# Performance work log

Measured on AMD Instinct MI355X. Metric: run time of the kernel, lower is better.

Reference implementation:

```python
import jax, jax.numpy as jnp
import numpy as np

INPUT_SIZE = 1024
HIDDEN_SIZE = 1024
BATCH = 4096


def setup_inputs() -> dict:
    key = jax.random.key(0)
    ks = jax.random.split(key, 16)
    s_in = 1.0 / np.sqrt(INPUT_SIZE)
    s_h = 1.0 / np.sqrt(HIDDEN_SIZE)
    inp = {
        "incoming": jax.random.normal(ks[0], (BATCH, INPUT_SIZE), jnp.float32),
        "old_h": jax.random.normal(ks[1], (BATCH, HIDDEN_SIZE), jnp.float32),
        "old_c": jax.random.normal(ks[2], (BATCH, HIDDEN_SIZE), jnp.float32),
    }
    # torch nn.Linear weights: [out, in]; y = x @ W.T + b
    names = ["i", "o", "f", "c"]
    for j, n in enumerate(names):
        inp[f"w_{n}"] = jax.random.normal(ks[3 + 3 * j], (HIDDEN_SIZE, INPUT_SIZE), jnp.float32) * s_in
        inp[f"b_{n}"] = jax.random.normal(ks[4 + 3 * j], (HIDDEN_SIZE,), jnp.float32) * s_in
        inp[f"u_{n}"] = jax.random.normal(ks[5 + 3 * j], (HIDDEN_SIZE, HIDDEN_SIZE), jnp.float32) * s_h
    return inp


def reference(incoming, old_h, old_c, w_i, b_i, u_i, w_o, b_o, u_o, w_f, b_f, u_f, w_c, b_c, u_c):
    # Concatenate the 4 input->gate and 4 hidden->gate matrices into two
    # fused GEMMs (same math as the 8 separate Linear calls).
    W = jnp.concatenate([w_i, w_o, w_f, w_c], axis=0)   # [4H, I]
    U = jnp.concatenate([u_i, u_o, u_f, u_c], axis=0)   # [4H, H]
    b = jnp.concatenate([b_i, b_o, b_f, b_c], axis=0)   # [4H]
    gates = incoming @ W.T + old_h @ U.T + b            # [B, 4H]
    gi, go, gf, gc = jnp.split(gates, 4, axis=-1)
    i = jax.nn.sigmoid(gi)
    o = jax.nn.sigmoid(go)
    f = jax.nn.sigmoid(gf)
    c_tilde = jnp.tanh(gc)
    new_c = f * old_c + i * c_tilde
    new_h = o * jnp.tanh(new_c)
    return (new_h, new_c)
```

## Files before the change

### kernel.cpp

```cpp
#include <hip/hip_runtime.h>

typedef __bf16 bf16x8 __attribute__((ext_vector_type(8)));
typedef float f32x4 __attribute__((ext_vector_type(4)));

#define B_  4096
#define IN_ 1024
#define H_  1024
#define KD  2048
#define ND  4096

__device__ __forceinline__ unsigned short f2bf(float f) {
    union { float f; unsigned u; } v; v.f = f;
    unsigned r = v.u + 0x7FFFu + ((v.u >> 16) & 1u);
    return (unsigned short)(r >> 16);
}
__device__ __forceinline__ float bf2f(unsigned short u) {
    union { unsigned u; float f; } v; v.u = ((unsigned)u) << 16; return v.f;
}

__global__ __launch_bounds__(256) void pack_z(const float* __restrict__ x,
                                              const float* __restrict__ h,
                                              unsigned short* __restrict__ Z) {
    int idx = (blockIdx.x * 256 + threadIdx.x) * 4;
    int m = idx >> 11;
    int k = idx & (KD - 1);
    const float* src = (k < IN_) ? (x + (size_t)m * IN_ + k)
                                 : (h + (size_t)m * H_ + (k - IN_));
    float4 v = *(const float4*)src;
    ushort4 o;
    o.x = f2bf(v.x); o.y = f2bf(v.y); o.z = f2bf(v.z); o.w = f2bf(v.w);
    *(ushort4*)(Z + idx) = o;
}

__global__ __launch_bounds__(256) void pack_v(const float* __restrict__ wi, const float* __restrict__ ui,
                                              const float* __restrict__ wo, const float* __restrict__ uo,
                                              const float* __restrict__ wf, const float* __restrict__ uf,
                                              const float* __restrict__ wc, const float* __restrict__ uc,
                                              unsigned short* __restrict__ V) {
    int idx = (blockIdx.x * 256 + threadIdx.x) * 4;
    int n = idx >> 11;
    int k = idx & (KD - 1);
    int g = n >> 10;
    int r = n & (H_ - 1);
    const float* wg = (g == 0) ? wi : (g == 1) ? wo : (g == 2) ? wf : wc;
    const float* ug = (g == 0) ? ui : (g == 1) ? uo : (g == 2) ? uf : uc;
    const float* src = (k < IN_) ? (wg + (size_t)r * IN_ + k)
                                 : (ug + (size_t)r * H_ + (k - IN_));
    float4 v = *(const float4*)src;
    ushort4 o;
    o.x = f2bf(v.x); o.y = f2bf(v.y); o.z = f2bf(v.z); o.w = f2bf(v.w);
    *(ushort4*)(V + idx) = o;
}

__global__ __launch_bounds__(256) void gemm_bt(const unsigned short* __restrict__ Z,
                                               const unsigned short* __restrict__ V,
                                               unsigned short* __restrict__ G) {
    __shared__ unsigned short lA[128 * 64];
    __shared__ unsigned short lB[128 * 64];
    const int tid  = threadIdx.x;
    const int lane = tid & 63;
    const int w    = tid >> 6;
    const int wr   = w >> 1;
    const int wc   = w & 1;
    const int m0   = blockIdx.y * 128;
    const int n0   = blockIdx.x * 128;

    f32x4 acc[4][4];
#pragma unroll
    for (int i = 0; i < 4; ++i)
#pragma unroll
        for (int j = 0; j < 4; ++j) acc[i][j] = (f32x4){0.f, 0.f, 0.f, 0.f};

    const int lr = lane >> 3;
    const int lc = (lane & 7) * 8;
    const unsigned short* gA = Z + (size_t)(m0 + w * 32 + lr) * KD + lc;
    const unsigned short* gB = V + (size_t)(n0 + w * 32 + lr) * KD + lc;
    unsigned short* lAw = lA + w * 32 * 64;
    unsigned short* lBw = lB + w * 32 * 64;

    const int lm = lane & 15;
    const int kq = (lane >> 4) * 8;

    for (int k0 = 0; k0 < KD; k0 += 64) {
#pragma unroll
        for (int c = 0; c < 4; ++c) {
            __builtin_amdgcn_global_load_lds(
                (const __attribute__((address_space(1))) void*)(gA + (size_t)c * 8 * KD + k0),
                (__attribute__((address_space(3))) void*)(lAw + c * 512), 16, 0, 0);
            __builtin_amdgcn_global_load_lds(
                (const __attribute__((address_space(1))) void*)(gB + (size_t)c * 8 * KD + k0),
                (__attribute__((address_space(3))) void*)(lBw + c * 512), 16, 0, 0);
        }
        __syncthreads();
#pragma unroll
        for (int ks = 0; ks < 2; ++ks) {
            bf16x8 af[4], bf[4];
            const int kb = ks * 32 + kq;
#pragma unroll
            for (int i = 0; i < 4; ++i) {
                af[i] = *(const bf16x8*)(lA + (wr * 64 + i * 16 + lm) * 64 + kb);
                bf[i] = *(const bf16x8*)(lB + (wc * 64 + i * 16 + lm) * 64 + kb);
            }
#pragma unroll
            for (int mi = 0; mi < 4; ++mi)
#pragma unroll
                for (int ni = 0; ni < 4; ++ni)
                    acc[mi][ni] = __builtin_amdgcn_mfma_f32_16x16x32_bf16(
                        af[mi], bf[ni], acc[mi][ni], 0, 0, 0);
        }
        __syncthreads();
    }

#pragma unroll
    for (int mi = 0; mi < 4; ++mi)
#pragma unroll
        for (int ni = 0; ni < 4; ++ni)
#pragma unroll
            for (int v = 0; v < 4; ++v) {
                int row = m0 + wr * 64 + mi * 16 + (lane >> 4) * 4 + v;
                int col = n0 + wc * 64 + ni * 16 + lm;
                G[(size_t)row * ND + col] = f2bf(acc[mi][ni][v]);
            }
}

__global__ __launch_bounds__(256) void lstm_elt(const unsigned short* __restrict__ G,
                                                const float* __restrict__ oc,
                                                const float* __restrict__ bi,
                                                const float* __restrict__ bo,
                                                const float* __restrict__ bff,
                                                const float* __restrict__ bc,
                                                float* __restrict__ nh,
                                                float* __restrict__ nc) {
    int idx = (blockIdx.x * 256 + threadIdx.x) * 4;
    int m = idx >> 10;
    int h = idx & (H_ - 1);
    size_t gb = (size_t)m * ND + h;
    ushort4 g0 = *(const ushort4*)(G + gb);
    ushort4 g1 = *(const ushort4*)(G + gb + 1024);
    ushort4 g2 = *(const ushort4*)(G + gb + 2048);
    ushort4 g3 = *(const ushort4*)(G + gb + 3072);
    float4 vbi = *(const float4*)(bi + h);
    float4 vbo = *(const float4*)(bo + h);
    float4 vbf = *(const float4*)(bff + h);
    float4 vbc = *(const float4*)(bc + h);
    float4 voc = *(const float4*)(oc + idx);
    float4 rh, rc;
#define COMP(c_)                                                         \
    {                                                                    \
        float gi = bf2f(g0.c_) + vbi.c_;                                 \
        float go = bf2f(g1.c_) + vbo.c_;                                 \
        float gf = bf2f(g2.c_) + vbf.c_;                                 \
        float gc = bf2f(g3.c_) + vbc.c_;                                 \
        float iv = 1.f / (1.f + __expf(-gi));                            \
        float ov = 1.f / (1.f + __expf(-go));                            \
        float fv = 1.f / (1.f + __expf(-gf));                            \
        float ct = 1.f - 2.f / (__expf(2.f * gc) + 1.f);                 \
        float cv = fv * voc.c_ + iv * ct;                                \
        float th = 1.f - 2.f / (__expf(2.f * cv) + 1.f);                 \
        rc.c_ = cv; rh.c_ = ov * th;                                     \
    }
    COMP(x) COMP(y) COMP(z) COMP(w)
#undef COMP
    *(float4*)(nh + idx) = rh;
    *(float4*)(nc + idx) = rc;
}

extern "C" void kernel_launch(void* const* d_in, const int* in_sizes, int n_in,
                              void* d_out, int out_size, void* d_ws, size_t ws_size,
                              hipStream_t stream) {
    const float* incoming = (const float*)d_in[0];
    const float* old_h    = (const float*)d_in[1];
    const float* old_c    = (const float*)d_in[2];
    const float* w_i = (const float*)d_in[3];
    const float* b_i = (const float*)d_in[4];
    const float* u_i = (const float*)d_in[5];
    const float* w_o = (const float*)d_in[6];
    const float* b_o = (const float*)d_in[7];
    const float* u_o = (const float*)d_in[8];
    const float* w_f = (const float*)d_in[9];
    const float* b_f = (const float*)d_in[10];
    const float* u_f = (const float*)d_in[11];
    const float* w_c = (const float*)d_in[12];
    const float* b_c = (const float*)d_in[13];
    const float* u_c = (const float*)d_in[14];

    unsigned short* Z = (unsigned short*)d_ws;
    unsigned short* V = Z + (size_t)B_ * KD;
    unsigned short* G = V + (size_t)ND * KD;

    pack_z<<<(B_ * KD / 4) / 256, 256, 0, stream>>>(incoming, old_h, Z);
    pack_v<<<((size_t)ND * KD / 4) / 256, 256, 0, stream>>>(
        w_i, u_i, w_o, u_o, w_f, u_f, w_c, u_c, V);
    gemm_bt<<<dim3(ND / 128, B_ / 128), 256, 0, stream>>>(Z, V, G);
    lstm_elt<<<(B_ * H_ / 4) / 256, 256, 0, stream>>>(
        G, old_c, b_i, b_o, b_f, b_c,
        (float*)d_out, (float*)d_out + (size_t)B_ * H_);
}
```

Before: 248.6 us.

## Fuse LSTM gate epilogue into GEMM with interleaved weight rows and LDS swizzle

Reorders the packed weight matrix so the four gates for each hidden unit sit in adjacent columns. The GEMM epilogue can then exchange accumulators across lanes with shuffles and compute new_h and new_c directly. This removes the bf16 gate buffer write and read and the separate elementwise launch. An XOR swizzle on the LDS tile layout is also added to cut bank conflicts on fragment reads. The tradeoffs are uncoalesced scalar old_c loads and output stores in the epilogue, plus extra shuffle work.

Measured after the change: 227.4 us. -8.5%, faster.

```diff
diff --git a/kernel.cpp b/kernel.cpp
--- a/kernel.cpp
+++ b/kernel.cpp
@@ -13,9 +13,6 @@
     union { float f; unsigned u; } v; v.f = f;
     unsigned r = v.u + 0x7FFFu + ((v.u >> 16) & 1u);
     return (unsigned short)(r >> 16);
-}
-__device__ __forceinline__ float bf2f(unsigned short u) {
-    union { unsigned u; float f; } v; v.u = ((unsigned)u) << 16; return v.f;
 }
 
 __global__ __launch_bounds__(256) void pack_z(const float* __restrict__ x,
@@ -40,8 +37,8 @@
     int idx = (blockIdx.x * 256 + threadIdx.x) * 4;
     int n = idx >> 11;
     int k = idx & (KD - 1);
-    int g = n >> 10;
-    int r = n & (H_ - 1);
+    int g = n & 3;
+    int r = n >> 2;
     const float* wg = (g == 0) ? wi : (g == 1) ? wo : (g == 2) ? wf : wc;
     const float* ug = (g == 0) ? ui : (g == 1) ? uo : (g == 2) ? uf : uc;
     const float* src = (k < IN_) ? (wg + (size_t)r * IN_ + k)
@@ -52,9 +49,15 @@
     *(ushort4*)(V + idx) = o;
 }
 
-__global__ __launch_bounds__(256) void gemm_bt(const unsigned short* __restrict__ Z,
-                                               const unsigned short* __restrict__ V,
-                                               unsigned short* __restrict__ G) {
+__global__ __launch_bounds__(256) void gemm_lstm(const unsigned short* __restrict__ Z,
+                                                 const unsigned short* __restrict__ V,
+                                                 const float* __restrict__ oc,
+                                                 const float* __restrict__ bi,
+                                                 const float* __restrict__ bo,
+                                                 const float* __restrict__ bff,
+                                                 const float* __restrict__ bc,
+                                                 float* __restrict__ nh,
+                                                 float* __restrict__ nc) {
     __shared__ unsigned short lA[128 * 64];
     __shared__ unsigned short lB[128 * 64];
     const int tid  = threadIdx.x;
@@ -72,7 +75,7 @@
         for (int j = 0; j < 4; ++j) acc[i][j] = (f32x4){0.f, 0.f, 0.f, 0.f};
 
     const int lr = lane >> 3;
-    const int lc = (lane & 7) * 8;
+    const int lc = ((lane & 7) ^ lr) * 8;
     const unsigned short* gA = Z + (size_t)(m0 + w * 32 + lr) * KD + lc;
     const unsigned short* gB = V + (size_t)(n0 + w * 32 + lr) * KD + lc;
     unsigned short* lAw = lA + w * 32 * 64;
@@ -95,11 +98,12 @@
 #pragma unroll
         for (int ks = 0; ks < 2; ++ks) {
             bf16x8 af[4], bf[4];
-            const int kb = ks * 32 + kq;
+            const int cb = ks * 4 + (lane >> 4);
+            const int sw = (cb ^ (lm & 7)) * 8;
 #pragma unroll
             for (int i = 0; i < 4; ++i) {
-                af[i] = *(const bf16x8*)(lA + (wr * 64 + i * 16 + lm) * 64 + kb);
-                bf[i] = *(const bf16x8*)(lB + (wc * 64 + i * 16 + lm) * 64 + kb);
+                af[i] = *(const bf16x8*)(lA + (wr * 64 + i * 16 + lm) * 64 + sw);
+                bf[i] = *(const bf16x8*)(lB + (wc * 64 + i * 16 + lm) * 64 + sw);
             }
 #pragma unroll
             for (int mi = 0; mi < 4; ++mi)
@@ -111,58 +115,43 @@
         __syncthreads();
     }
 
+    const int a  = lane >> 4;
+    const int b  = (lane >> 2) & 3;
+    const int g  = lane & 3;
+    const int h0 = blockIdx.x * 32 + wc * 16;
+    const int rowb = m0 + wr * 64 + 4 * a + g;
+
 #pragma unroll
-    for (int mi = 0; mi < 4; ++mi)
+    for (int ni = 0; ni < 4; ++ni) {
+        const int h = h0 + ni * 4 + b;
+        const float vbi = bi[h];
+        const float vbo = bo[h];
+        const float vbf = bff[h];
+        const float vbc = bc[h];
 #pragma unroll
-        for (int ni = 0; ni < 4; ++ni)
+        for (int mi = 0; mi < 4; ++mi) {
+            float recv[4];
 #pragma unroll
-            for (int v = 0; v < 4; ++v) {
-                int row = m0 + wr * 64 + mi * 16 + (lane >> 4) * 4 + v;
-                int col = n0 + wc * 64 + ni * 16 + lm;
-                G[(size_t)row * ND + col] = f2bf(acc[mi][ni][v]);
+            for (int t = 0; t < 4; ++t) {
+                float x = acc[mi][ni][(g ^ t) & 3];
+                recv[t] = __shfl_xor(x, t, 64);
             }
-}
-
-__global__ __launch_bounds__(256) void lstm_elt(const unsigned short* __restrict__ G,
-                                                const float* __restrict__ oc,
-                                                const float* __restrict__ bi,
-                                                const float* __restrict__ bo,
-                                                const float* __restrict__ bff,
-                                                const float* __restrict__ bc,
-                                                float* __restrict__ nh,
-                                                float* __restrict__ nc) {
-    int idx = (blockIdx.x * 256 + threadIdx.x) * 4;
-    int m = idx >> 10;
-    int h = idx & (H_ - 1);
-    size_t gb = (size_t)m * ND + h;
-    ushort4 g0 = *(const ushort4*)(G + gb);
-    ushort4 g1 = *(const ushort4*)(G + gb + 1024);
-    ushort4 g2 = *(const ushort4*)(G + gb + 2048);
-    ushort4 g3 = *(const ushort4*)(G + gb + 3072);
-    float4 vbi = *(const float4*)(bi + h);
-    float4 vbo = *(const float4*)(bo + h);
-    float4 vbf = *(const float4*)(bff + h);
-    float4 vbc = *(const float4*)(bc + h);
-    float4 voc = *(const float4*)(oc + idx);
-    float4 rh, rc;
-#define COMP(c_)                                                         \
-    {                                                                    \
-        float gi = bf2f(g0.c_) + vbi.c_;                                 \
-        float go = bf2f(g1.c_) + vbo.c_;                                 \
-        float gf = bf2f(g2.c_) + vbf.c_;                                 \
-        float gc = bf2f(g3.c_) + vbc.c_;                                 \
-        float iv = 1.f / (1.f + __expf(-gi));                            \
-        float ov = 1.f / (1.f + __expf(-go));                            \
-        float fv = 1.f / (1.f + __expf(-gf));                            \
-        float ct = 1.f - 2.f / (__expf(2.f * gc) + 1.f);                 \
-        float cv = fv * voc.c_ + iv * ct;                                \
-        float th = 1.f - 2.f / (__expf(2.f * cv) + 1.f);                 \
-        rc.c_ = cv; rh.c_ = ov * th;                                     \
+            float gi = recv[g] + vbi;
+            float go = recv[g ^ 1] + vbo;
+            float gf = recv[g ^ 2] + vbf;
+            float gc = recv[g ^ 3] + vbc;
+            const int row = rowb + mi * 16;
+            const size_t off = (size_t)row * H_ + h;
+            float iv = 1.f / (1.f + __expf(-gi));
+            float ov = 1.f / (1.f + __expf(-go));
+            float fv = 1.f / (1.f + __expf(-gf));
+            float ct = 1.f - 2.f / (__expf(2.f * gc) + 1.f);
+            float cv = fv * oc[off] + iv * ct;
+            float th = 1.f - 2.f / (__expf(2.f * cv) + 1.f);
+            nc[off] = cv;
+            nh[off] = ov * th;
+        }
     }
-    COMP(x) COMP(y) COMP(z) COMP(w)
-#undef COMP
-    *(float4*)(nh + idx) = rh;
-    *(float4*)(nc + idx) = rc;
 }
 
 extern "C" void kernel_launch(void* const* d_in, const int* in_sizes, int n_in,
@@ -186,13 +175,11 @@
 
     unsigned short* Z = (unsigned short*)d_ws;
     unsigned short* V = Z + (size_t)B_ * KD;
-    unsigned short* G = V + (size_t)ND * KD;
 
     pack_z<<<(B_ * KD / 4) / 256, 256, 0, stream>>>(incoming, old_h, Z);
     pack_v<<<((size_t)ND * KD / 4) / 256, 256, 0, stream>>>(
         w_i, u_i, w_o, u_o, w_f, u_f, w_c, u_c, V);
-    gemm_bt<<<dim3(ND / 128, B_ / 128), 256, 0, stream>>>(Z, V, G);
-    lstm_elt<<<(B_ * H_ / 4) / 256, 256, 0, stream>>>(
-        G, old_c, b_i, b_o, b_f, b_c,
+    gemm_lstm<<<dim3(ND / 128, B_ / 128), 256, 0, stream>>>(
+        Z, V, old_c, b_i, b_o, b_f, b_c,
         (float*)d_out, (float*)d_out + (size_t)B_ * H_);
 }
```
